# Optimization experiments

Hardware: AMD Instinct MI355X
Metric: run time of the kernel (lower is better)

The kernel has to match this reference:

```python
import jax, jax.numpy as jnp
import numpy as np

POOL = 7  # pool_size from init_kwargs


def _roi_bilinear(img, roi):
    """Crop roi=(x,y,w,h) from img [H,W,C] and bilinearly resize to POOLxPOOL.
    Matches tf.image.resize_images bilinear, align_corners=False:
    src_coord = dst_coord * (in_size / out_size), neighbors clamped to crop."""
    x0, y0, w, h = roi[0], roi[1], roi[2], roi[3]
    grid = jnp.arange(POOL, dtype=jnp.float32)
    ys = y0.astype(jnp.float32) + grid * (h.astype(jnp.float32) / POOL)
    xs = x0.astype(jnp.float32) + grid * (w.astype(jnp.float32) / POOL)
    ty = jnp.floor(ys).astype(jnp.int32)
    tx = jnp.floor(xs).astype(jnp.int32)
    fy = (ys - ty.astype(jnp.float32))[:, None, None]
    fx = (xs - tx.astype(jnp.float32))[None, :, None]
    by = jnp.minimum(ty + 1, y0 + h - 1)  # clamp to crop's last row
    bx = jnp.minimum(tx + 1, x0 + w - 1)  # clamp to crop's last col
    v00 = img[ty[:, None], tx[None, :]]  # [P,P,C]
    v01 = img[ty[:, None], bx[None, :]]
    v10 = img[by[:, None], tx[None, :]]
    v11 = img[by[:, None], bx[None, :]]
    top = (1.0 - fx) * v00 + fx * v01
    bot = (1.0 - fx) * v10 + fx * v11
    return (1.0 - fy) * top + fy * bot


def setup_inputs() -> dict:
    key = jax.random.key(0)
    k1, k2, k3 = jax.random.split(key, 3)
    img = jax.random.normal(k1, (1, 200, 200, 512), dtype=jnp.float32)
    xy = jax.random.randint(k2, (1, 300, 2), 0, 64, dtype=jnp.int32)
    wh = jax.random.randint(k3, (1, 300, 2), 1, 64, dtype=jnp.int32)
    rois = jnp.concatenate([xy, wh], axis=-1)  # (x, y, w, h)
    return {"img": img, "rois": rois}


def reference(img, rois):
    # img [1,H,W,C], rois [1,R,4] int32 -> [1,R,POOL,POOL,C]
    out = jax.vmap(lambda r: _roi_bilinear(img[0], r))(rois[0])
    return out[None]
```

## Files before the change

kernel.cpp:

```cpp
#include <hip/hip_runtime.h>


#define IMG_W 200
#define NCH   512
#define NPOS  49

__global__ __launch_bounds__(128) void roi_bilinear_kernel(
    const float* __restrict__ img,
    const int*   __restrict__ rois,
    float*       __restrict__ out)
{
    int bid = blockIdx.x;
    int r   = bid / NPOS;
    int rem = bid - r * NPOS;
    int py  = rem / 7;
    int px  = rem - py * 7;

    int x0 = rois[4 * r + 0];
    int y0 = rois[4 * r + 1];
    int w  = rois[4 * r + 2];
    int h  = rois[4 * r + 3];

    float sy = __fdiv_rn((float)h, 7.0f);
    float sx = __fdiv_rn((float)w, 7.0f);
    float ys = __fadd_rn((float)y0, __fmul_rn((float)py, sy));
    float xs = __fadd_rn((float)x0, __fmul_rn((float)px, sx));

    int ty = (int)floorf(ys);
    int tx = (int)floorf(xs);
    float fy = __fsub_rn(ys, (float)ty);
    float fx = __fsub_rn(xs, (float)tx);

    int by = min(ty + 1, y0 + h - 1);
    int bx = min(tx + 1, x0 + w - 1);

    const float4* p00 = (const float4*)(img + (size_t)(ty * IMG_W + tx) * NCH);
    const float4* p01 = (const float4*)(img + (size_t)(ty * IMG_W + bx) * NCH);
    const float4* p10 = (const float4*)(img + (size_t)(by * IMG_W + tx) * NCH);
    const float4* p11 = (const float4*)(img + (size_t)(by * IMG_W + bx) * NCH);
    float4*       po  = (float4*)(out + (size_t)bid * NCH);

    int t = threadIdx.x;
    float4 v00 = p00[t];
    float4 v01 = p01[t];
    float4 v10 = p10[t];
    float4 v11 = p11[t];

    float gx = 1.0f - fx;
    float gy = 1.0f - fy;

    float4 o;
    o.x = gy * (gx * v00.x + fx * v01.x) + fy * (gx * v10.x + fx * v11.x);
    o.y = gy * (gx * v00.y + fx * v01.y) + fy * (gx * v10.y + fx * v11.y);
    o.z = gy * (gx * v00.z + fx * v01.z) + fy * (gx * v10.z + fx * v11.z);
    o.w = gy * (gx * v00.w + fx * v01.w) + fy * (gx * v10.w + fx * v11.w);
    po[t] = o;
}

extern "C" void kernel_launch(void* const* d_in, const int* in_sizes, int n_in,
                              void* d_out, int out_size, void* d_ws, size_t ws_size,
                              hipStream_t stream)
{
    const float* img  = (const float*)d_in[0];
    const int*   rois = (const int*)d_in[1];
    float*       out  = (float*)d_out;

    const int nroi = in_sizes[1] / 4;
    dim3 grid(nroi * NPOS);
    dim3 block(128);
    roi_bilinear_kernel<<<grid, block, 0, stream>>>(img, rois, out);
}
```

Measured before the change: 122.5 us.

## Process a full output row per block with batched loads

Each block now computes all seven output columns of one pooled row instead of a single output position, cutting the grid by a factor of seven. All 28 float4 gathers are issued up front into registers before any arithmetic, which raises memory-level parallelism per thread and amortizes ROI parameter loads and index math. The ROI record is read with one int4 load. In exchange there are fewer blocks (2100) and higher register pressure, which may reduce occupancy on a large GPU.

New measurement: 123.3 us. About the same (+0.7%).

```diff
diff --git a/kernel.cpp b/kernel.cpp
--- a/kernel.cpp
+++ b/kernel.cpp
@@ -3,7 +3,8 @@
 
 #define IMG_W 200
 #define NCH   512
-#define NPOS  49
+#define POOL  7
+#define V4PP  (NCH / 4)
 
 __global__ __launch_bounds__(128) void roi_bilinear_kernel(
     const float* __restrict__ img,
@@ -11,50 +12,60 @@
     float*       __restrict__ out)
 {
     int bid = blockIdx.x;
-    int r   = bid / NPOS;
-    int rem = bid - r * NPOS;
-    int py  = rem / 7;
-    int px  = rem - py * 7;
+    int r   = bid / POOL;
+    int py  = bid - r * POOL;
 
-    int x0 = rois[4 * r + 0];
-    int y0 = rois[4 * r + 1];
-    int w  = rois[4 * r + 2];
-    int h  = rois[4 * r + 3];
+    int4 rv = *(const int4*)(rois + 4 * r);
+    int x0 = rv.x, y0 = rv.y, w = rv.z, h = rv.w;
 
     float sy = __fdiv_rn((float)h, 7.0f);
     float sx = __fdiv_rn((float)w, 7.0f);
+
     float ys = __fadd_rn((float)y0, __fmul_rn((float)py, sy));
-    float xs = __fadd_rn((float)x0, __fmul_rn((float)px, sx));
+    int   ty = (int)floorf(ys);
+    float fy = __fsub_rn(ys, (float)ty);
+    int   by = min(ty + 1, y0 + h - 1);
 
-    int ty = (int)floorf(ys);
-    int tx = (int)floorf(xs);
-    float fy = __fsub_rn(ys, (float)ty);
-    float fx = __fsub_rn(xs, (float)tx);
+    const float4* imgv = (const float4*)img;
+    int t = threadIdx.x;
+    int rowTo = ty * IMG_W * V4PP + t;
+    int rowBo = by * IMG_W * V4PP + t;
 
-    int by = min(ty + 1, y0 + h - 1);
-    int bx = min(tx + 1, x0 + w - 1);
+    int   txi[POOL], bxi[POOL];
+    float fx[POOL];
+    #pragma unroll
+    for (int px = 0; px < POOL; ++px) {
+        float xs = __fadd_rn((float)x0, __fmul_rn((float)px, sx));
+        int   tx = (int)floorf(xs);
+        fx[px]  = __fsub_rn(xs, (float)tx);
+        txi[px] = tx;
+        bxi[px] = min(tx + 1, x0 + w - 1);
+    }
 
-    const float4* p00 = (const float4*)(img + (size_t)(ty * IMG_W + tx) * NCH);
-    const float4* p01 = (const float4*)(img + (size_t)(ty * IMG_W + bx) * NCH);
-    const float4* p10 = (const float4*)(img + (size_t)(by * IMG_W + tx) * NCH);
-    const float4* p11 = (const float4*)(img + (size_t)(by * IMG_W + bx) * NCH);
-    float4*       po  = (float4*)(out + (size_t)bid * NCH);
+    float4 v00[POOL], v01[POOL], v10[POOL], v11[POOL];
+    #pragma unroll
+    for (int px = 0; px < POOL; ++px) {
+        v00[px] = imgv[rowTo + txi[px] * V4PP];
+        v01[px] = imgv[rowTo + bxi[px] * V4PP];
+        v10[px] = imgv[rowBo + txi[px] * V4PP];
+        v11[px] = imgv[rowBo + bxi[px] * V4PP];
+    }
 
-    int t = threadIdx.x;
-    float4 v00 = p00[t];
-    float4 v01 = p01[t];
-    float4 v10 = p10[t];
-    float4 v11 = p11[t];
+    float gy = 1.0f - fy;
+    float4* outv   = (float4*)out;
+    int     outIdx = (r * 49 + py * POOL) * V4PP + t;
 
-    float gx = 1.0f - fx;
-    float gy = 1.0f - fy;
-
-    float4 o;
-    o.x = gy * (gx * v00.x + fx * v01.x) + fy * (gx * v10.x + fx * v11.x);
-    o.y = gy * (gx * v00.y + fx * v01.y) + fy * (gx * v10.y + fx * v11.y);
-    o.z = gy * (gx * v00.z + fx * v01.z) + fy * (gx * v10.z + fx * v11.z);
-    o.w = gy * (gx * v00.w + fx * v01.w) + fy * (gx * v10.w + fx * v11.w);
-    po[t] = o;
+    #pragma unroll
+    for (int px = 0; px < POOL; ++px) {
+        float f = fx[px];
+        float g = 1.0f - f;
+        float4 o;
+        o.x = gy * (g * v00[px].x + f * v01[px].x) + fy * (g * v10[px].x + f * v11[px].x);
+        o.y = gy * (g * v00[px].y + f * v01[px].y) + fy * (g * v10[px].y + f * v11[px].y);
+        o.z = gy * (g * v00[px].z + f * v01[px].z) + fy * (g * v10[px].z + f * v11[px].z);
+        o.w = gy * (g * v00[px].w + f * v01[px].w) + fy * (g * v10[px].w + f * v11[px].w);
+        outv[outIdx + px * V4PP] = o;
+    }
 }
 
 extern "C" void kernel_launch(void* const* d_in, const int* in_sizes, int n_in,
@@ -66,7 +77,7 @@
     float*       out  = (float*)d_out;
 
     const int nroi = in_sizes[1] / 4;
-    dim3 grid(nroi * NPOS);
+    dim3 grid(nroi * POOL);
     dim3 block(128);
     roi_bilinear_kernel<<<grid, block, 0, stream>>>(img, rois, out);
 }
```
